# Performance work log

Measured on AMD Instinct MI355X. Metric: run time of the kernel, lower is better.

## Reference

```python
import jax, jax.numpy as jnp
import numpy as np

B, C, H, W_SP = 4, 64, 64, 64
CI = C // 2  # inter_channels = 32
DEPTH = 64
EPS = 1e-5


def conv2d(x, w, b, pad=0, dil=1):
    out = jax.lax.conv_general_dilated(
        x, w, window_strides=(1, 1),
        padding=[(pad, pad), (pad, pad)],
        rhs_dilation=(dil, dil),
        dimension_numbers=('NCHW', 'OIHW', 'NCHW'))
    return out + b[None, :, None, None]


def setup_inputs() -> dict:
    key = jax.random.key(0)
    ks = iter(jax.random.split(key, 32))
    nrm = lambda shp, s=0.01: jax.random.normal(next(ks), shp, jnp.float32) * s
    inp = {
        'x': jax.random.normal(next(ks), (B, C, H, W_SP), jnp.float32),
        # NonlocalBlock params (init: normal(0, 0.01), bias 0)
        'g_w': nrm((CI, C, 1, 1)), 'g_b': jnp.zeros((CI,), jnp.float32),
        'theta_w': nrm((CI, C, 1, 1)), 'theta_b': jnp.zeros((CI,), jnp.float32),
        'phi_w': nrm((CI, C, 1, 1)), 'phi_b': jnp.zeros((CI,), jnp.float32),
        'Wz_w': nrm((C, CI, 1, 1)), 'Wz_b': jnp.zeros((C,), jnp.float32),
        'bn_g': jax.random.normal(next(ks), (C,), jnp.float32),  # normal_(W[1].weight, 0) -> std 1
        'bn_b': jnp.zeros((C,), jnp.float32),
        # ASPP params (torch default kaiming init approximated by small normals)
        'a_mean_w': nrm((DEPTH, C, 1, 1), 0.05), 'a_mean_b': jnp.zeros((DEPTH,), jnp.float32),
        'a1_w': nrm((DEPTH, C, 1, 1), 0.05), 'a1_b': jnp.zeros((DEPTH,), jnp.float32),
        'a3_w': nrm((DEPTH, C, 3, 3), 0.02), 'a3_b': jnp.zeros((DEPTH,), jnp.float32),
        'a5_w': nrm((DEPTH, C, 3, 3), 0.02), 'a5_b': jnp.zeros((DEPTH,), jnp.float32),
        'a7_w': nrm((DEPTH, C, 3, 3), 0.02), 'a7_b': jnp.zeros((DEPTH,), jnp.float32),
        'out_w': nrm((DEPTH, DEPTH * 5, 1, 1), 0.02), 'out_b': jnp.zeros((DEPTH,), jnp.float32),
    }
    return inp


def _forward(x, g_w, g_b, theta_w, theta_b, phi_w, phi_b, Wz_w, Wz_b, bn_g, bn_b,
             a_mean_w, a_mean_b, a1_w, a1_b, a3_w, a3_b, a5_w, a5_b, a7_w, a7_b,
             out_w, out_b):
    b, c, h, w = x.shape
    n = h * w
    # ---- NonlocalBlock: global self-attention ----
    g_x = conv2d(x, g_w, g_b).reshape(b, CI, n).transpose(0, 2, 1)       # [B,N,Ci]
    theta_x = conv2d(x, theta_w, theta_b).reshape(b, CI, n).transpose(0, 2, 1)  # [B,N,Ci]
    phi_x = conv2d(x, phi_w, phi_b).reshape(b, CI, n)                    # [B,Ci,N]
    f = jnp.einsum('bqc,bck->bqk', theta_x, phi_x)                       # [B,N,N]
    f_div_C = jax.nn.softmax(f, axis=2)
    y = jnp.einsum('bqk,bkc->bqc', f_div_C, g_x)                         # [B,N,Ci]
    y = y.transpose(0, 2, 1).reshape(b, CI, h, w)
    wy = conv2d(y, Wz_w, Wz_b)
    # BatchNorm (eval: running_mean=0, running_var=1)
    wy = wy * (bn_g / jnp.sqrt(1.0 + EPS))[None, :, None, None] + bn_b[None, :, None, None]
    z = wy + x
    # ---- ASPP ----
    img = jnp.mean(z, axis=(2, 3), keepdims=True)                        # [B,C,1,1]
    img = conv2d(img, a_mean_w, a_mean_b)                                # [B,D,1,1]
    img = jnp.broadcast_to(img, (b, DEPTH, h, w))  # bilinear upsample of 1x1 is constant
    b1 = conv2d(z, a1_w, a1_b)
    b3 = conv2d(z, a3_w, a3_b, pad=3, dil=3)
    b5 = conv2d(z, a5_w, a5_b, pad=5, dil=5)
    b7 = conv2d(z, a7_w, a7_b, pad=7, dil=7)
    cat = jnp.concatenate([img, b1, b3, b5, b7], axis=1)                 # [B,5D,H,W]
    return conv2d(cat, out_w, out_b)                                     # [B,D,H,W]


def reference(x, g_w, g_b, theta_w, theta_b, phi_w, phi_b, Wz_w, Wz_b, bn_g, bn_b,
              a_mean_w, a_mean_b, a1_w, a1_b, a3_w, a3_b, a5_w, a5_b, a7_w, a7_b,
              out_w, out_b):
    return _forward(x, g_w, g_b, theta_w, theta_b, phi_w, phi_b, Wz_w, Wz_b, bn_g, bn_b,
                    a_mean_w, a_mean_b, a1_w, a1_b, a3_w, a3_b, a5_w, a5_b, a7_w, a7_b,
                    out_w, out_b)
```

## Files before the change

kernel.cpp:

```cpp
#include <hip/hip_runtime.h>


typedef __attribute__((ext_vector_type(8))) short bf16x8;
typedef __attribute__((ext_vector_type(4))) short s16x4;
typedef __attribute__((ext_vector_type(4))) float f32x4;

#define MFMA(a, b, c) __builtin_amdgcn_mfma_f32_16x16x32_bf16((a), (b), (c), 0, 0, 0)

#if __has_builtin(__builtin_amdgcn_exp2f)
#define EXP2(x) __builtin_amdgcn_exp2f(x)
#else
#define EXP2(x) exp2f(x)
#endif

__device__ static inline short f2bf(float f) {
  union { float f; unsigned u; } v; v.f = f;
  unsigned r = v.u + 0x7fffu + ((v.u >> 16) & 1u);
  return (short)(r >> 16);
}
__device__ static inline s16x4 pk4(f32x4 v) {
  s16x4 r; r.x = f2bf(v.x); r.y = f2bf(v.y); r.z = f2bf(v.z); r.w = f2bf(v.w);
  return r;
}
__device__ static inline unsigned pk2(float f0, float f1) {
  union { float f; unsigned u; } a, b; a.f = f0; b.f = f1;
  return __builtin_amdgcn_perm(b.u, a.u, 0x07060302u);
}
__device__ static inline float unlo(unsigned d) {
  union { unsigned u; float f; } v; v.u = d << 16; return v.f;
}
__device__ static inline float unhi(unsigned d) {
  union { unsigned u; float f; } v; v.u = d & 0xffff0000u; return v.f;
}
__device__ static inline unsigned fasu(float f) {
  union { float f; unsigned u; } v; v.f = f; return v.u;
}
__device__ static inline float uasf(unsigned u) {
  union { unsigned u; float f; } v; v.u = u; return v.f;
}
__device__ static inline f32x4 exp24(f32x4 v) {
  f32x4 r; r.x = EXP2(v.x); r.y = EXP2(v.y); r.z = EXP2(v.z); r.w = EXP2(v.w);
  return r;
}

#define QF_PER_B 131072
#define ZPB      389376
#define LOG2E    1.4426950408889634f

__global__ __launch_bounds__(256) void k_proj(
    const float* __restrict__ x,
    const float* __restrict__ tw, const float* __restrict__ tb,
    const float* __restrict__ pw, const float* __restrict__ pb,
    const float* __restrict__ gw, const float* __restrict__ gb,
    const float* __restrict__ Wz_w, const float* __restrict__ Wz_b,
    const float* __restrict__ bn_g, const float* __restrict__ bn_b,
    const float* __restrict__ out_w, const float* __restrict__ out_b,
    const float* __restrict__ a1_w, const float* __restrict__ a3_w,
    const float* __restrict__ a5_w, const float* __restrict__ a7_w,
    const float* __restrict__ a1_b, const float* __restrict__ a3_b,
    const float* __restrict__ a5_b, const float* __restrict__ a7_b,
    const float* __restrict__ am_w,
    unsigned short* __restrict__ thetaB, unsigned short* __restrict__ phiB,
    unsigned short* __restrict__ gB, unsigned short* __restrict__ WzF,
    float* __restrict__ bias2, float* __restrict__ zpart,
    unsigned* __restrict__ zp, unsigned short* __restrict__ Wfrag,
    float* __restrict__ am_wT, float* __restrict__ owT0,
    float* __restrict__ cbias) {
  __shared__ union {
    struct { float wlT[2048]; float bl[32]; } qkv;
    struct { float wsm[4096]; float osm[64 * 65]; } prep;
  } sm;
  int blk = blockIdx.x, t = threadIdx.x;
  if (blk < 384) {
    int proj = blk >> 7, r = blk & 127;
    int b = r & 3, pt = r >> 2;
    const float* w    = proj == 0 ? tw : (proj == 1 ? pw : gw);
    const float* bias = proj == 0 ? tb : (proj == 1 ? pb : gb);
    for (int i = t; i < 2048; i += 256)
      sm.qkv.wlT[(i & 63) * 32 + (i >> 6)] = w[i];
    if (t < 32) sm.qkv.bl[t] = bias[t];
    __syncthreads();
    int px = pt * 128 + (t & 127), tci = t >> 7;
    const float* xp = x + b*64*4096 + px;
    float acc[16];
    #pragma unroll
    for (int i = 0; i < 16; ++i) acc[i] = sm.qkv.bl[tci*16 + i];
    for (int c0 = 0; c0 < 64; c0 += 16) {
      float xv[16];
      #pragma unroll
      for (int k = 0; k < 16; ++k) xv[k] = xp[(c0 + k)*4096];
      #pragma unroll
      for (int k = 0; k < 16; ++k) {
        const float* wr = &sm.qkv.wlT[(c0 + k)*32 + tci*16];
        #pragma unroll
        for (int j = 0; j < 4; ++j) {
          f32x4 wv = *(const f32x4*)(wr + j*4);
          acc[j*4 + 0] += wv.x * xv[k];
          acc[j*4 + 1] += wv.y * xv[k];
          acc[j*4 + 2] += wv.z * xv[k];
          acc[j*4 + 3] += wv.w * xv[k];
        }
      }
    }
    if (proj == 0) {
      #pragma unroll
      for (int i = 0; i < 16; ++i) acc[i] *= LOG2E;
    }
    if (proj < 2) {
      unsigned short* base = (proj == 0 ? thetaB : phiB) + b*QF_PER_B
                             + (px >> 4)*512 + (px & 15)*8;
      #pragma unroll
      for (int qq = 0; qq < 2; ++qq) {
        bf16x8 v;
        #pragma unroll
        for (int j = 0; j < 8; ++j) v[j] = f2bf(acc[qq*8 + j]);
        *(bf16x8*)(base + (tci*2 + qq)*128) = v;
      }
    } else {
      unsigned short* base = gB + b*QF_PER_B + (px >> 5)*1024
                             + ((px & 31) >> 3)*128 + (px & 7) + tci*512;
      #pragma unroll
      for (int ci = 0; ci < 16; ++ci)
        base[ci*8] = (unsigned short)f2bf(acc[ci]);
    }
  } else if (blk == 384) {
    int ct = t >> 6, lane = t & 63, quad = lane >> 4, l15 = lane & 15;
    int c = ct * 16 + l15;
    float s = bn_g[c] * rsqrtf(1.f + 1e-5f);
    bf16x8 v;
    #pragma unroll
    for (int j = 0; j < 8; ++j) v[j] = f2bf(s * Wz_w[c * 32 + quad * 8 + j]);
    *(bf16x8*)(WzF + (ct * 64 + lane) * 8) = v;
    #pragma unroll
    for (int i = 0; i < 8; ++i) zpart[i*256 + t] = 0.f;
    if (t < 64) {
      float s2 = bn_g[t] * rsqrtf(1.f + 1e-5f);
      bias2[t] = s2 * Wz_b[t] + bn_b[t];
    }
  } else if (blk < 1381) {
    int hb = blk - 385;
    int b = hb / 249, loc = hb - b * 249;
    int i = loc * 256 + t;
    if (i >= 63616) return;
    int px = i >> 5, dw = i & 31;
    int row, col;
    if (px < 1092) {
      int r = px / 78; col = px - r * 78;
      row = (r < 7) ? r : r + 64;
    } else {
      int j = px - 1092;
      int r = j / 14; int c = j - r * 14;
      row = r + 7; col = (c < 7) ? c : c + 64;
    }
    zp[b * (ZPB / 2) + (row * 78 + col) * 32 + dw] = 0u;
  } else if (blk < 1409) {
    int tap = blk - 1381;
    const float* w; int goff, kyx = 0, ksq = 9;
    if (tap == 0)      { w = a1_w; goff = 64;  ksq = 1; }
    else if (tap < 10) { w = a3_w; goff = 128; kyx = tap - 1; }
    else if (tap < 19) { w = a5_w; goff = 192; kyx = tap - 10; }
    else               { w = a7_w; goff = 256; kyx = tap - 19; }
    for (int i = t; i < 4096; i += 256) {
      sm.prep.wsm[i] = w[i * ksq + kyx];
      int d = i >> 6, m = i & 63;
      sm.prep.osm[d * 65 + m] = out_w[d * 320 + goff + m];
    }
    __syncthreads();
    int dt = t >> 6, lane = t & 63, quad = lane >> 4, l15 = lane & 15;
    int d = dt * 16 + l15;
    float acc[16];
    #pragma unroll
    for (int k = 0; k < 16; ++k) acc[k] = 0.f;
    const float* orow = sm.prep.osm + d * 65;
    int c0 = quad * 8;
    for (int m = 0; m < 64; ++m) {
      float o = orow[m];
      const float* wr = sm.prep.wsm + m * 64 + c0;
      #pragma unroll
      for (int cc = 0; cc < 2; ++cc)
        #pragma unroll
        for (int j = 0; j < 8; ++j)
          acc[cc * 8 + j] += o * wr[cc * 32 + j];
    }
    #pragma unroll
    for (int cc = 0; cc < 2; ++cc) {
      bf16x8 v;
      #pragma unroll
      for (int j = 0; j < 8; ++j) v[j] = f2bf(acc[cc * 8 + j]);
      *(bf16x8*)(Wfrag + (((tap * 4 + dt) * 2 + cc) * 64 + lane) * 8) = v;
    }
  } else {
    for (int i = t; i < 4096; i += 256) {
      int d = i >> 6, c = i & 63;
      am_wT[c * 64 + d] = am_w[i];
      owT0[c * 64 + d] = out_w[d * 320 + c];
    }
    if (t < 64) {
      float r = out_b[t];
      const float* ow = out_w + t * 320;
      for (int m = 0; m < 64; ++m)
        r += ow[64 + m] * a1_b[m] + ow[128 + m] * a3_b[m]
           + ow[192 + m] * a5_b[m] + ow[256 + m] * a7_b[m];
      cbias[t] = r;
    }
  }
}

__global__ __launch_bounds__(512, 8) void k_attn(
    const unsigned short* __restrict__ thetaB, const unsigned short* __restrict__ phiB,
    const unsigned short* __restrict__ gB, const unsigned short* __restrict__ WzF,
    const float* __restrict__ bias2, const float* __restrict__ x,
    unsigned short* __restrict__ z_pad, float* __restrict__ zpart) {
  __shared__ struct {
    unsigned ypk[8][5][64];
    __align__(16) unsigned short plds[8][576];
  } sm;
  int blk = blockIdx.x;
  int xcd = blk & 7;
  int b = xcd >> 1;
  int qblk = ((xcd & 1) << 7) | (blk >> 3);
  int tid = threadIdx.x;
  int kh = tid >> 6, lane = tid & 63, quad = lane >> 4, l15 = lane & 15;
  const bf16x8* thB = (const bf16x8*)(thetaB + b*QF_PER_B);
  const bf16x8* phF = (const bf16x8*)(phiB + b*QF_PER_B);
  const bf16x8* gF  = (const bf16x8*)(gB + b*QF_PER_B);
  bf16x8 th = thB[qblk*64 + lane];
  bf16x8 ones;
  #pragma unroll
  for (int j = 0; j < 8; ++j) ones[j] = (short)0x3F80;
  const f32x4 z4 = {0.f, 0.f, 0.f, 0.f};
  f32x4 acc0 = z4, acc1 = z4, accL = z4;
  unsigned short* pl = &sm.plds[kh][0];
  unsigned short* rp = pl + l15*36 + quad*4;
  const unsigned short* qp = pl + l15*36 + quad*8;
  int kt0 = kh*16;
  int tb0 = kt0*128 + lane;
  bf16x8 pf0 = phF[tb0], pf1 = phF[tb0 + 64];
  for (int kt = kt0; kt < kt0 + 16; ++kt) {
    bf16x8 cp0 = pf0, cp1 = pf1;
    bf16x8 gf0 = gF[kt*128 + lane];
    bf16x8 gf1 = gF[kt*128 + lane + 64];
    if (kt + 1 < kt0 + 16) {
      int tb = (kt + 1)*128 + lane;
      pf0 = phF[tb]; pf1 = phF[tb + 64];
    }
    f32x4 s0 = MFMA(cp0, th, z4);
    f32x4 s1 = MFMA(cp1, th, z4);
    f32x4 p0 = exp24(s0), p1 = exp24(s1);
    uint2 w0; w0.x = pk2(p0.x, p0.y); w0.y = pk2(p0.z, p0.w);
    uint2 w1; w1.x = pk2(p1.x, p1.y); w1.y = pk2(p1.z, p1.w);
    *(uint2*)(rp)      = w0;
    *(uint2*)(rp + 16) = w1;
    uint2 a0 = *(const uint2*)(qp);
    uint2 a1 = *(const uint2*)(qp + 4);
    union { unsigned u[4]; bf16x8 v; } pb;
    pb.u[0] = a0.x; pb.u[1] = a0.y; pb.u[2] = a1.x; pb.u[3] = a1.y;
    acc0 = MFMA(gf0, pb.v, acc0);
    acc1 = MFMA(gf1, pb.v, acc1);
    accL = MFMA(ones, pb.v, accL);
  }
  {
    unsigned* yp = &sm.ypk[kh][0][lane];
    yp[0*64] = pk2(acc0.x, acc0.y);
    yp[1*64] = pk2(acc0.z, acc0.w);
    yp[2*64] = pk2(acc1.x, acc1.y);
    yp[3*64] = pk2(acc1.z, acc1.w);
    yp[4*64] = fasu(accL.x);
  }
  __syncthreads();
  if (kh >= 4) return;
  int ct = kh;
  f32x4 a0 = z4, a1 = z4;
  float l = 0.f;
  #pragma unroll
  for (int k = 0; k < 8; ++k) {
    const unsigned* q = &sm.ypk[k][0][lane];
    unsigned d0v = q[0], d1v = q[64], d2v = q[128], d3v = q[192];
    a0.x += unlo(d0v); a0.y += unhi(d0v); a0.z += unlo(d1v); a0.w += unhi(d1v);
    a1.x += unlo(d2v); a1.y += unhi(d2v); a1.z += unlo(d3v); a1.w += unhi(d3v);
    l += uasf(q[256]);
  }
  float rl = 1.f / l;
  a0 *= rl; a1 *= rl;
  unsigned short* yl = &sm.plds[ct][0];
  *(s16x4*)(yl + l15*36 + quad*4)      = pk4(a0);
  *(s16x4*)(yl + l15*36 + 16 + quad*4) = pk4(a1);
  bf16x8 y = *(const bf16x8*)(yl + l15*36 + quad*8);
  bf16x8 wf = ((const bf16x8*)WzF)[ct*64 + lane];
  f32x4 zq = MFMA(wf, y, z4);
  int c0 = ct*16 + quad*4;
  f32x4 b2 = *(const f32x4*)(bias2 + c0);
  int q = qblk*16 + l15;
  const float* xp = x + (b*64 + c0)*4096 + q;
  f32x4 s;
  s.x = zq.x + b2.x + xp[0];
  s.y = zq.y + b2.y + xp[4096];
  s.z = zq.z + b2.z + xp[8192];
  s.w = zq.w + b2.w + xp[12288];
  int h = q >> 6, w = q & 63;
  *(s16x4*)(z_pad + b*ZPB + ((h + 7)*78 + (w + 7))*64 + c0) = pk4(s);
  f32x4 zs = s;
  #pragma unroll
  for (int m = 1; m < 16; m <<= 1) {
    zs.x += __shfl_xor(zs.x, m);
    zs.y += __shfl_xor(zs.y, m);
    zs.z += __shfl_xor(zs.z, m);
    zs.w += __shfl_xor(zs.w, m);
  }
  if (l15 == 0) {
    float* zd = zpart + (qblk & 7)*256 + b*64 + c0;
    atomicAdd(zd + 0, zs.x);
    atomicAdd(zd + 1, zs.y);
    atomicAdd(zd + 2, zs.z);
    atomicAdd(zd + 3, zs.w);
  }
}

__global__ __launch_bounds__(256, 4) void k_conv(
    const unsigned short* __restrict__ z_pad, const unsigned short* __restrict__ Wfrag,
    const float* __restrict__ zpart, const float* __restrict__ am_wT,
    const float* __restrict__ am_b, const float* __restrict__ owT0,
    const float* __restrict__ cbias, float* __restrict__ out) {
  static constexpr int DYt[28] = {0, -3,-3,-3,0,0,0,3,3,3,
                                     -5,-5,-5,0,0,0,5,5,5,
                                     -7,-7,-7,0,0,0,7,7,7};
  static constexpr int DXt[28] = {0, -3,0,3,-3,0,3,-3,0,3,
                                     -5,0,5,-5,0,5,-5,0,5,
                                     -7,0,7,-7,0,7,-7,0,7};
  int blk = blockIdx.x;
  int xcd = blk & 7, idx = blk >> 3;
  int h = xcd*8 + (idx & 7);
  int rest = idx >> 3;
  int b = rest & 3, wh = rest >> 2;
  int tid = threadIdx.x;
  int wave = tid >> 6, lane = tid & 63, quad = lane >> 4, l15 = lane & 15;
  int dt2 = wave >> 1, cf = wave & 1;
  float zm = 0.f;
  #pragma unroll
  for (int p = 0; p < 8; ++p) zm += zpart[p*256 + b*64 + lane];
  float zml = zm * (1.f / 4096.f);
  float img = am_b[lane];
  for (int c = 0; c < 64; ++c) img += am_wT[c*64 + lane] * __shfl(zml, c);
  float cbd = cbias[lane];
  for (int dd = 0; dd < 64; ++dd) cbd += owT0[dd*64 + lane] * __shfl(img, dd);
  const unsigned short* zb = z_pad + b*ZPB + ((h + 7)*78 + 7)*64 + quad*8;
  const bf16x8* wfp = (const bf16x8*)Wfrag + lane;
  int d0 = dt2*2 + 0, d1 = dt2*2 + 1;
  const f32x4 z4 = {0.f, 0.f, 0.f, 0.f};
  f32x4 acc0 = z4, acc1 = z4;
  int col = ((wh*2 + cf)*16 + l15)*64;
  bf16x8 zq[4], wq0[4], wq1[4];
  #pragma unroll
  for (int p = 0; p < 4; ++p) {
    int tap = p >> 1, cc = p & 1;
    zq[p] = *(const bf16x8*)(zb + (DYt[tap]*78 + DXt[tap])*64 + cc*32 + col);
    wq0[p] = wfp[((tap*4 + d0)*2 + cc)*64];
    wq1[p] = wfp[((tap*4 + d1)*2 + cc)*64];
  }
  #pragma unroll
  for (int idx2 = 0; idx2 < 56; ++idx2) {
    int slot = idx2 & 3;
    bf16x8 zc = zq[slot], wc0 = wq0[slot], wc1 = wq1[slot];
    if (idx2 + 4 < 56) {
      int ntap = (idx2 + 4) >> 1, ncc = (idx2 + 4) & 1;
      zq[slot] = *(const bf16x8*)(zb + (DYt[ntap]*78 + DXt[ntap])*64 + ncc*32 + col);
      wq0[slot] = wfp[((ntap*4 + d0)*2 + ncc)*64];
      wq1[slot] = wfp[((ntap*4 + d1)*2 + ncc)*64];
    }
    acc0 = MFMA(wc0, zc, acc0);
    acc1 = MFMA(wc1, zc, acc1);
  }
  int dd0 = d0*16 + quad*4, dd1 = d1*16 + quad*4;
  f32x4 cb0v, cb1v;
  cb0v.x = __shfl(cbd, dd0 + 0); cb0v.y = __shfl(cbd, dd0 + 1);
  cb0v.z = __shfl(cbd, dd0 + 2); cb0v.w = __shfl(cbd, dd0 + 3);
  cb1v.x = __shfl(cbd, dd1 + 0); cb1v.y = __shfl(cbd, dd1 + 1);
  cb1v.z = __shfl(cbd, dd1 + 2); cb1v.w = __shfl(cbd, dd1 + 3);
  acc0 += cb0v; acc1 += cb1v;
  float* ob = out + b*262144 + h*64;
  int w0 = (wh*2 + cf)*16 + l15;
  ob[(dd0 + 0)*4096 + w0] = acc0.x;
  ob[(dd0 + 1)*4096 + w0] = acc0.y;
  ob[(dd0 + 2)*4096 + w0] = acc0.z;
  ob[(dd0 + 3)*4096 + w0] = acc0.w;
  ob[(dd1 + 0)*4096 + w0] = acc1.x;
  ob[(dd1 + 1)*4096 + w0] = acc1.y;
  ob[(dd1 + 2)*4096 + w0] = acc1.z;
  ob[(dd1 + 3)*4096 + w0] = acc1.w;
}

extern "C" void kernel_launch(void* const* d_in, const int* in_sizes, int n_in,
                              void* d_out, int out_size, void* d_ws, size_t ws_size,
                              hipStream_t stream) {
  const float* x    = (const float*)d_in[0];
  const float* g_w  = (const float*)d_in[1];
  const float* g_b  = (const float*)d_in[2];
  const float* th_w = (const float*)d_in[3];
  const float* th_b = (const float*)d_in[4];
  const float* ph_w = (const float*)d_in[5];
  const float* ph_b = (const float*)d_in[6];
  const float* Wz_w = (const float*)d_in[7];
  const float* Wz_b = (const float*)d_in[8];
  const float* bn_g = (const float*)d_in[9];
  const float* bn_b = (const float*)d_in[10];
  const float* am_w = (const float*)d_in[11];
  const float* am_b = (const float*)d_in[12];
  const float* a1_w = (const float*)d_in[13];
  const float* a1_b = (const float*)d_in[14];
  const float* a3_w = (const float*)d_in[15];
  const float* a3_b = (const float*)d_in[16];
  const float* a5_w = (const float*)d_in[17];
  const float* a5_b = (const float*)d_in[18];
  const float* a7_w = (const float*)d_in[19];
  const float* a7_b = (const float*)d_in[20];
  const float* out_w = (const float*)d_in[21];
  const float* out_b = (const float*)d_in[22];
  float* out = (float*)d_out;
  char* ws = (char*)d_ws;
  unsigned short* thetaB = (unsigned short*)(ws + 0);
  unsigned short* phiB   = (unsigned short*)(ws + 1048576);
  unsigned short* gB     = (unsigned short*)(ws + 2097152);
  unsigned short* z_pad  = (unsigned short*)(ws + 3145728);
  unsigned short* Wfrag  = (unsigned short*)(ws + 6260736);
  unsigned short* WzF    = (unsigned short*)(ws + 6490112);
  float* bias2           = (float*)(ws + 6495232);
  float* am_wT           = (float*)(ws + 6495488);
  float* owT0            = (float*)(ws + 6511872);
  float* cbias           = (float*)(ws + 6528256);
  float* zpart           = (float*)(ws + 6528512);

  k_proj<<<dim3(1410), dim3(256), 0, stream>>>(
      x, th_w, th_b, ph_w, ph_b, g_w, g_b, Wz_w, Wz_b, bn_g, bn_b,
      out_w, out_b, a1_w, a3_w, a5_w, a7_w, a1_b, a3_b, a5_b, a7_b, am_w,
      thetaB, phiB, gB, WzF, bias2, zpart,
      (unsigned*)z_pad, Wfrag, am_wT, owT0, cbias);
  k_attn<<<dim3(1024), dim3(512), 0, stream>>>(thetaB, phiB, gB, WzF, bias2, x,
                                               z_pad, zpart);
  k_conv<<<dim3(512), dim3(256), 0, stream>>>(z_pad, Wfrag, zpart, am_wT, am_b,
                                              owT0, cbias, out);
}
```

Measured before the change: 162.5 us.

## Process two query tiles per attention block to reuse phi/g fragments

Each k_attn block now handles 32 queries (two 16-query tiles) instead of 16. The loaded phi and g key fragments feed MFMAs for both tiles, which halves global key/value traffic per query, and the g loads are now software-prefetched along with phi. The grid is halved to 512 blocks, LDS buffers double, and launch bounds drop to 4 waves per SIMD. This trades lower occupancy and parallelism for higher arithmetic intensity.

```diff
diff --git a/kernel.cpp b/kernel.cpp
--- a/kernel.cpp
+++ b/kernel.cpp
@@ -206,100 +206,136 @@
   }
 }
 
-__global__ __launch_bounds__(512, 8) void k_attn(
+__global__ __launch_bounds__(512, 4) void k_attn(
     const unsigned short* __restrict__ thetaB, const unsigned short* __restrict__ phiB,
     const unsigned short* __restrict__ gB, const unsigned short* __restrict__ WzF,
     const float* __restrict__ bias2, const float* __restrict__ x,
     unsigned short* __restrict__ z_pad, float* __restrict__ zpart) {
   __shared__ struct {
-    unsigned ypk[8][5][64];
-    __align__(16) unsigned short plds[8][576];
+    unsigned ypk[8][10][64];
+    __align__(16) unsigned short plds[8][1152];
   } sm;
   int blk = blockIdx.x;
   int xcd = blk & 7;
   int b = xcd >> 1;
-  int qblk = ((xcd & 1) << 7) | (blk >> 3);
+  int qblk = ((xcd & 1) << 6) | (blk >> 3);
   int tid = threadIdx.x;
   int kh = tid >> 6, lane = tid & 63, quad = lane >> 4, l15 = lane & 15;
   const bf16x8* thB = (const bf16x8*)(thetaB + b*QF_PER_B);
   const bf16x8* phF = (const bf16x8*)(phiB + b*QF_PER_B);
   const bf16x8* gF  = (const bf16x8*)(gB + b*QF_PER_B);
-  bf16x8 th = thB[qblk*64 + lane];
+  bf16x8 th0 = thB[(qblk*2 + 0)*64 + lane];
+  bf16x8 th1 = thB[(qblk*2 + 1)*64 + lane];
   bf16x8 ones;
   #pragma unroll
   for (int j = 0; j < 8; ++j) ones[j] = (short)0x3F80;
   const f32x4 z4 = {0.f, 0.f, 0.f, 0.f};
-  f32x4 acc0 = z4, acc1 = z4, accL = z4;
+  f32x4 acc00 = z4, acc01 = z4, acc10 = z4, acc11 = z4;
+  f32x4 accL0 = z4, accL1 = z4;
   unsigned short* pl = &sm.plds[kh][0];
-  unsigned short* rp = pl + l15*36 + quad*4;
-  const unsigned short* qp = pl + l15*36 + quad*8;
+  unsigned short* r0p = pl + l15*36 + quad*4;
+  unsigned short* r1p = pl + 576 + l15*36 + quad*4;
+  const unsigned short* q0p = pl + l15*36 + quad*8;
+  const unsigned short* q1p = pl + 576 + l15*36 + quad*8;
   int kt0 = kh*16;
   int tb0 = kt0*128 + lane;
   bf16x8 pf0 = phF[tb0], pf1 = phF[tb0 + 64];
+  bf16x8 gf0 = gF[tb0],  gf1 = gF[tb0 + 64];
   for (int kt = kt0; kt < kt0 + 16; ++kt) {
-    bf16x8 cp0 = pf0, cp1 = pf1;
-    bf16x8 gf0 = gF[kt*128 + lane];
-    bf16x8 gf1 = gF[kt*128 + lane + 64];
+    bf16x8 cp0 = pf0, cp1 = pf1, cg0 = gf0, cg1 = gf1;
     if (kt + 1 < kt0 + 16) {
       int tb = (kt + 1)*128 + lane;
       pf0 = phF[tb]; pf1 = phF[tb + 64];
-    }
-    f32x4 s0 = MFMA(cp0, th, z4);
-    f32x4 s1 = MFMA(cp1, th, z4);
-    f32x4 p0 = exp24(s0), p1 = exp24(s1);
-    uint2 w0; w0.x = pk2(p0.x, p0.y); w0.y = pk2(p0.z, p0.w);
-    uint2 w1; w1.x = pk2(p1.x, p1.y); w1.y = pk2(p1.z, p1.w);
-    *(uint2*)(rp)      = w0;
-    *(uint2*)(rp + 16) = w1;
-    uint2 a0 = *(const uint2*)(qp);
-    uint2 a1 = *(const uint2*)(qp + 4);
-    union { unsigned u[4]; bf16x8 v; } pb;
-    pb.u[0] = a0.x; pb.u[1] = a0.y; pb.u[2] = a1.x; pb.u[3] = a1.y;
-    acc0 = MFMA(gf0, pb.v, acc0);
-    acc1 = MFMA(gf1, pb.v, acc1);
-    accL = MFMA(ones, pb.v, accL);
+      gf0 = gF[tb];  gf1 = gF[tb + 64];
+    }
+    f32x4 s00 = MFMA(cp0, th0, z4);
+    f32x4 s10 = MFMA(cp1, th0, z4);
+    f32x4 s01 = MFMA(cp0, th1, z4);
+    f32x4 s11 = MFMA(cp1, th1, z4);
+    f32x4 p00 = exp24(s00), p10 = exp24(s10), p01 = exp24(s01), p11 = exp24(s11);
+    uint2 w0; w0.x = pk2(p00.x, p00.y); w0.y = pk2(p00.z, p00.w);
+    uint2 w1; w1.x = pk2(p10.x, p10.y); w1.y = pk2(p10.z, p10.w);
+    uint2 w2; w2.x = pk2(p01.x, p01.y); w2.y = pk2(p01.z, p01.w);
+    uint2 w3; w3.x = pk2(p11.x, p11.y); w3.y = pk2(p11.z, p11.w);
+    *(uint2*)(r0p)      = w0;
+    *(uint2*)(r0p + 16) = w1;
+    *(uint2*)(r1p)      = w2;
+    *(uint2*)(r1p + 16) = w3;
+    uint2 a0 = *(const uint2*)(q0p);
+    uint2 a1 = *(const uint2*)(q0p + 4);
+    uint2 b0 = *(const uint2*)(q1p);
+    uint2 b1 = *(const uint2*)(q1p + 4);
+    union { unsigned u[4]; bf16x8 v; } pb0c, pb1c;
+    pb0c.u[0] = a0.x; pb0c.u[1] = a0.y; pb0c.u[2] = a1.x; pb0c.u[3] = a1.y;
+    pb1c.u[0] = b0.x; pb1c.u[1] = b0.y; pb1c.u[2] = b1.x; pb1c.u[3] = b1.y;
+    acc00 = MFMA(cg0, pb0c.v, acc00);
+    acc01 = MFMA(cg1, pb0c.v, acc01);
+    acc10 = MFMA(cg0, pb1c.v, acc10);
+    acc11 = MFMA(cg1, pb1c.v, acc11);
+    accL0 = MFMA(ones, pb0c.v, accL0);
+    accL1 = MFMA(ones, pb1c.v, accL1);
   }
   {
     unsigned* yp = &sm.ypk[kh][0][lane];
-    yp[0*64] = pk2(acc0.x, acc0.y);
-    yp[1*64] = pk2(acc0.z, acc0.w);
-    yp[2*64] = pk2(acc1.x, acc1.y);
-    yp[3*64] = pk2(acc1.z, acc1.w);
-    yp[4*64] = fasu(accL.x);
+    yp[0*64] = pk2(acc00.x, acc00.y);
+    yp[1*64] = pk2(acc00.z, acc00.w);
+    yp[2*64] = pk2(acc01.x, acc01.y);
+    yp[3*64] = pk2(acc01.z, acc01.w);
+    yp[4*64] = pk2(acc10.x, acc10.y);
+    yp[5*64] = pk2(acc10.z, acc10.w);
+    yp[6*64] = pk2(acc11.x, acc11.y);
+    yp[7*64] = pk2(acc11.z, acc11.w);
+    yp[8*64] = fasu(accL0.x);
+    yp[9*64] = fasu(accL1.x);
   }
   __syncthreads();
   if (kh >= 4) return;
   int ct = kh;
-  f32x4 a0 = z4, a1 = z4;
-  float l = 0.f;
+  f32x4 a00 = z4, a01 = z4, a10 = z4, a11 = z4;
+  float l0 = 0.f, l1 = 0.f;
   #pragma unroll
   for (int k = 0; k < 8; ++k) {
     const unsigned* q = &sm.ypk[k][0][lane];
     unsigned d0v = q[0], d1v = q[64], d2v = q[128], d3v = q[192];
-    a0.x += unlo(d0v); a0.y += unhi(d0v); a0.z += unlo(d1v); a0.w += unhi(d1v);
-    a1.x += unlo(d2v); a1.y += unhi(d2v); a1.z += unlo(d3v); a1.w += unhi(d3v);
-    l += uasf(q[256]);
-  }
-  float rl = 1.f / l;
-  a0 *= rl; a1 *= rl;
-  unsigned short* yl = &sm.plds[ct][0];
-  *(s16x4*)(yl + l15*36 + quad*4)      = pk4(a0);
-  *(s16x4*)(yl + l15*36 + 16 + quad*4) = pk4(a1);
-  bf16x8 y = *(const bf16x8*)(yl + l15*36 + quad*8);
+    unsigned d4v = q[256], d5v = q[320], d6v = q[384], d7v = q[448];
+    a00.x += unlo(d0v); a00.y += unhi(d0v); a00.z += unlo(d1v); a00.w += unhi(d1v);
+    a01.x += unlo(d2v); a01.y += unhi(d2v); a01.z += unlo(d3v); a01.w += unhi(d3v);
+    a10.x += unlo(d4v); a10.y += unhi(d4v); a10.z += unlo(d5v); a10.w += unhi(d5v);
+    a11.x += unlo(d6v); a11.y += unhi(d6v); a11.z += unlo(d7v); a11.w += unhi(d7v);
+    l0 += uasf(q[512]); l1 += uasf(q[576]);
+  }
+  float r0 = 1.f / l0, r1 = 1.f / l1;
+  a00 *= r0; a01 *= r0; a10 *= r1; a11 *= r1;
+  unsigned short* yl = &sm.plds[0][0] + ct*1280;
+  *(s16x4*)(yl + l15*40 + quad*4)             = pk4(a00);
+  *(s16x4*)(yl + l15*40 + 16 + quad*4)        = pk4(a01);
+  *(s16x4*)(yl + (16 + l15)*40 + quad*4)      = pk4(a10);
+  *(s16x4*)(yl + (16 + l15)*40 + 16 + quad*4) = pk4(a11);
+  bf16x8 y0 = *(const bf16x8*)(yl + l15*40 + quad*8);
+  bf16x8 y1 = *(const bf16x8*)(yl + (16 + l15)*40 + quad*8);
   bf16x8 wf = ((const bf16x8*)WzF)[ct*64 + lane];
-  f32x4 zq = MFMA(wf, y, z4);
+  f32x4 zq0 = MFMA(wf, y0, z4);
+  f32x4 zq1 = MFMA(wf, y1, z4);
   int c0 = ct*16 + quad*4;
   f32x4 b2 = *(const f32x4*)(bias2 + c0);
-  int q = qblk*16 + l15;
-  const float* xp = x + (b*64 + c0)*4096 + q;
-  f32x4 s;
-  s.x = zq.x + b2.x + xp[0];
-  s.y = zq.y + b2.y + xp[4096];
-  s.z = zq.z + b2.z + xp[8192];
-  s.w = zq.w + b2.w + xp[12288];
-  int h = q >> 6, w = q & 63;
-  *(s16x4*)(z_pad + b*ZPB + ((h + 7)*78 + (w + 7))*64 + c0) = pk4(s);
-  f32x4 zs = s;
+  int q0i = qblk * 32;
+  const float* xp0 = x + (b*64 + c0)*4096 + q0i + l15;
+  f32x4 s0, s1;
+  s0.x = zq0.x + b2.x + xp0[0];
+  s0.y = zq0.y + b2.y + xp0[4096];
+  s0.z = zq0.z + b2.z + xp0[8192];
+  s0.w = zq0.w + b2.w + xp0[12288];
+  s1.x = zq1.x + b2.x + xp0[16];
+  s1.y = zq1.y + b2.y + xp0[4096 + 16];
+  s1.z = zq1.z + b2.z + xp0[8192 + 16];
+  s1.w = zq1.w + b2.w + xp0[12288 + 16];
+  {
+    int q = q0i + l15, h = q >> 6, w = q & 63;
+    *(s16x4*)(z_pad + b*ZPB + ((h + 7)*78 + (w + 7))*64 + c0) = pk4(s0);
+    q = q0i + 16 + l15; h = q >> 6; w = q & 63;
+    *(s16x4*)(z_pad + b*ZPB + ((h + 7)*78 + (w + 7))*64 + c0) = pk4(s1);
+  }
+  f32x4 zs = s0 + s1;
   #pragma unroll
   for (int m = 1; m < 16; m <<= 1) {
     zs.x += __shfl_xor(zs.x, m);
@@ -434,8 +470,8 @@
       out_w, out_b, a1_w, a3_w, a5_w, a7_w, a1_b, a3_b, a5_b, a7_b, am_w,
       thetaB, phiB, gB, WzF, bias2, zpart,
       (unsigned*)z_pad, Wfrag, am_wT, owT0, cbias);
-  k_attn<<<dim3(1024), dim3(512), 0, stream>>>(thetaB, phiB, gB, WzF, bias2, x,
-                                               z_pad, zpart);
+  k_attn<<<dim3(512), dim3(512), 0, stream>>>(thetaB, phiB, gB, WzF, bias2, x,
+                                              z_pad, zpart);
   k_conv<<<dim3(512), dim3(256), 0, stream>>>(z_pad, Wfrag, zpart, am_wT, am_b,
                                               owT0, cbias, out);
 }
```

Result: faster. 157.4 us (median of 2 runs) (-3.2%).

## Process four query tiles per attention block to reuse phi and g key loads

Applied to the files above, without the earlier changes.

Each attention block now handles 64 queries (four 16-query tiles) instead of 16, so every loaded phi/g key fragment feeds four score and accumulate MFMA sets. The grid shrinks from 1024 to 256 blocks and launch bounds drop to 2 waves/SIMD to make room for the larger accumulator state. The intent is to cut global/L2 traffic for keys and values by a factor of four. In exchange, parallelism falls to 256 blocks on a 256-CU part, and register and LDS pressure rise.

```diff
diff --git a/kernel.cpp b/kernel.cpp
--- a/kernel.cpp
+++ b/kernel.cpp
@@ -206,113 +206,147 @@
   }
 }
 
-__global__ __launch_bounds__(512, 8) void k_attn(
+struct WaveBuf {
+  union {
+    __align__(16) unsigned short plds[2304];
+    unsigned ypk[20][64];
+  };
+};
+__global__ __launch_bounds__(512, 2) void k_attn(
     const unsigned short* __restrict__ thetaB, const unsigned short* __restrict__ phiB,
     const unsigned short* __restrict__ gB, const unsigned short* __restrict__ WzF,
     const float* __restrict__ bias2, const float* __restrict__ x,
     unsigned short* __restrict__ z_pad, float* __restrict__ zpart) {
   __shared__ struct {
-    unsigned ypk[8][5][64];
-    __align__(16) unsigned short plds[8][576];
+    WaveBuf w[8];
+    __align__(16) unsigned short ytr[4][2560];
   } sm;
   int blk = blockIdx.x;
   int xcd = blk & 7;
   int b = xcd >> 1;
-  int qblk = ((xcd & 1) << 7) | (blk >> 3);
+  int qblk = ((xcd & 1) << 5) | (blk >> 3);
   int tid = threadIdx.x;
   int kh = tid >> 6, lane = tid & 63, quad = lane >> 4, l15 = lane & 15;
   const bf16x8* thB = (const bf16x8*)(thetaB + b*QF_PER_B);
   const bf16x8* phF = (const bf16x8*)(phiB + b*QF_PER_B);
   const bf16x8* gF  = (const bf16x8*)(gB + b*QF_PER_B);
-  bf16x8 th = thB[qblk*64 + lane];
+  bf16x8 th[4];
+  #pragma unroll
+  for (int qt = 0; qt < 4; ++qt) th[qt] = thB[(qblk*4 + qt)*64 + lane];
   bf16x8 ones;
   #pragma unroll
   for (int j = 0; j < 8; ++j) ones[j] = (short)0x3F80;
   const f32x4 z4 = {0.f, 0.f, 0.f, 0.f};
-  f32x4 acc0 = z4, acc1 = z4, accL = z4;
-  unsigned short* pl = &sm.plds[kh][0];
-  unsigned short* rp = pl + l15*36 + quad*4;
-  const unsigned short* qp = pl + l15*36 + quad*8;
+  f32x4 acc[4][2], accL[4];
+  #pragma unroll
+  for (int qt = 0; qt < 4; ++qt) { acc[qt][0] = z4; acc[qt][1] = z4; accL[qt] = z4; }
+  unsigned short* pl = &sm.w[kh].plds[0];
   int kt0 = kh*16;
   int tb0 = kt0*128 + lane;
   bf16x8 pf0 = phF[tb0], pf1 = phF[tb0 + 64];
+  bf16x8 gf0 = gF[tb0],  gf1 = gF[tb0 + 64];
   for (int kt = kt0; kt < kt0 + 16; ++kt) {
-    bf16x8 cp0 = pf0, cp1 = pf1;
-    bf16x8 gf0 = gF[kt*128 + lane];
-    bf16x8 gf1 = gF[kt*128 + lane + 64];
+    bf16x8 cp0 = pf0, cp1 = pf1, cg0 = gf0, cg1 = gf1;
     if (kt + 1 < kt0 + 16) {
       int tb = (kt + 1)*128 + lane;
       pf0 = phF[tb]; pf1 = phF[tb + 64];
-    }
-    f32x4 s0 = MFMA(cp0, th, z4);
-    f32x4 s1 = MFMA(cp1, th, z4);
-    f32x4 p0 = exp24(s0), p1 = exp24(s1);
-    uint2 w0; w0.x = pk2(p0.x, p0.y); w0.y = pk2(p0.z, p0.w);
-    uint2 w1; w1.x = pk2(p1.x, p1.y); w1.y = pk2(p1.z, p1.w);
-    *(uint2*)(rp)      = w0;
-    *(uint2*)(rp + 16) = w1;
-    uint2 a0 = *(const uint2*)(qp);
-    uint2 a1 = *(const uint2*)(qp + 4);
-    union { unsigned u[4]; bf16x8 v; } pb;
-    pb.u[0] = a0.x; pb.u[1] = a0.y; pb.u[2] = a1.x; pb.u[3] = a1.y;
-    acc0 = MFMA(gf0, pb.v, acc0);
-    acc1 = MFMA(gf1, pb.v, acc1);
-    accL = MFMA(ones, pb.v, accL);
+      gf0 = gF[tb];  gf1 = gF[tb + 64];
+    }
+    #pragma unroll
+    for (int qt = 0; qt < 4; ++qt) {
+      f32x4 s0 = MFMA(cp0, th[qt], z4);
+      f32x4 s1 = MFMA(cp1, th[qt], z4);
+      f32x4 p0 = exp24(s0), p1 = exp24(s1);
+      uint2 w0; w0.x = pk2(p0.x, p0.y); w0.y = pk2(p0.z, p0.w);
+      uint2 w1; w1.x = pk2(p1.x, p1.y); w1.y = pk2(p1.z, p1.w);
+      unsigned short* rp = pl + qt*576 + l15*36 + quad*4;
+      *(uint2*)(rp)      = w0;
+      *(uint2*)(rp + 16) = w1;
+    }
+    #pragma unroll
+    for (int qt = 0; qt < 4; ++qt) {
+      const unsigned short* qp = pl + qt*576 + l15*36 + quad*8;
+      uint2 a0 = *(const uint2*)(qp);
+      uint2 a1 = *(const uint2*)(qp + 4);
+      union { unsigned u[4]; bf16x8 v; } pb;
+      pb.u[0] = a0.x; pb.u[1] = a0.y; pb.u[2] = a1.x; pb.u[3] = a1.y;
+      acc[qt][0] = MFMA(cg0, pb.v, acc[qt][0]);
+      acc[qt][1] = MFMA(cg1, pb.v, acc[qt][1]);
+      accL[qt]   = MFMA(ones, pb.v, accL[qt]);
+    }
   }
   {
-    unsigned* yp = &sm.ypk[kh][0][lane];
-    yp[0*64] = pk2(acc0.x, acc0.y);
-    yp[1*64] = pk2(acc0.z, acc0.w);
-    yp[2*64] = pk2(acc1.x, acc1.y);
-    yp[3*64] = pk2(acc1.z, acc1.w);
-    yp[4*64] = fasu(accL.x);
+    unsigned* yp = &sm.w[kh].ypk[0][lane];
+    #pragma unroll
+    for (int qt = 0; qt < 4; ++qt) {
+      yp[(qt*4 + 0)*64] = pk2(acc[qt][0].x, acc[qt][0].y);
+      yp[(qt*4 + 1)*64] = pk2(acc[qt][0].z, acc[qt][0].w);
+      yp[(qt*4 + 2)*64] = pk2(acc[qt][1].x, acc[qt][1].y);
+      yp[(qt*4 + 3)*64] = pk2(acc[qt][1].z, acc[qt][1].w);
+      yp[(16 + qt)*64]  = fasu(accL[qt].x);
+    }
   }
   __syncthreads();
   if (kh >= 4) return;
   int ct = kh;
-  f32x4 a0 = z4, a1 = z4;
-  float l = 0.f;
+  f32x4 a0[4], a1[4];
+  float l[4];
+  #pragma unroll
+  for (int qt = 0; qt < 4; ++qt) { a0[qt] = z4; a1[qt] = z4; l[qt] = 0.f; }
   #pragma unroll
   for (int k = 0; k < 8; ++k) {
-    const unsigned* q = &sm.ypk[k][0][lane];
-    unsigned d0v = q[0], d1v = q[64], d2v = q[128], d3v = q[192];
-    a0.x += unlo(d0v); a0.y += unhi(d0v); a0.z += unlo(d1v); a0.w += unhi(d1v);
-    a1.x += unlo(d2v); a1.y += unhi(d2v); a1.z += unlo(d3v); a1.w += unhi(d3v);
-    l += uasf(q[256]);
-  }
-  float rl = 1.f / l;
-  a0 *= rl; a1 *= rl;
-  unsigned short* yl = &sm.plds[ct][0];
-  *(s16x4*)(yl + l15*36 + quad*4)      = pk4(a0);
-  *(s16x4*)(yl + l15*36 + 16 + quad*4) = pk4(a1);
-  bf16x8 y = *(const bf16x8*)(yl + l15*36 + quad*8);
+    const unsigned* q = &sm.w[k].ypk[0][lane];
+    #pragma unroll
+    for (int qt = 0; qt < 4; ++qt) {
+      unsigned d0v = q[(qt*4 + 0)*64], d1v = q[(qt*4 + 1)*64];
+      unsigned d2v = q[(qt*4 + 2)*64], d3v = q[(qt*4 + 3)*64];
+      a0[qt].x += unlo(d0v); a0[qt].y += unhi(d0v);
+      a0[qt].z += unlo(d1v); a0[qt].w += unhi(d1v);
+      a1[qt].x += unlo(d2v); a1[qt].y += unhi(d2v);
+      a1[qt].z += unlo(d3v); a1[qt].w += unhi(d3v);
+      l[qt] += uasf(q[(16 + qt)*64]);
+    }
+  }
+  unsigned short* yl = &sm.ytr[ct][0];
+  #pragma unroll
+  for (int qt = 0; qt < 4; ++qt) {
+    float rl = 1.f / l[qt];
+    a0[qt] *= rl; a1[qt] *= rl;
+    *(s16x4*)(yl + (qt*16 + l15)*40 + quad*4)      = pk4(a0[qt]);
+    *(s16x4*)(yl + (qt*16 + l15)*40 + 16 + quad*4) = pk4(a1[qt]);
+  }
   bf16x8 wf = ((const bf16x8*)WzF)[ct*64 + lane];
-  f32x4 zq = MFMA(wf, y, z4);
   int c0 = ct*16 + quad*4;
   f32x4 b2 = *(const f32x4*)(bias2 + c0);
-  int q = qblk*16 + l15;
-  const float* xp = x + (b*64 + c0)*4096 + q;
-  f32x4 s;
-  s.x = zq.x + b2.x + xp[0];
-  s.y = zq.y + b2.y + xp[4096];
-  s.z = zq.z + b2.z + xp[8192];
-  s.w = zq.w + b2.w + xp[12288];
-  int h = q >> 6, w = q & 63;
-  *(s16x4*)(z_pad + b*ZPB + ((h + 7)*78 + (w + 7))*64 + c0) = pk4(s);
-  f32x4 zs = s;
+  f32x4 zsum = z4;
+  #pragma unroll
+  for (int qt = 0; qt < 4; ++qt) {
+    bf16x8 y = *(const bf16x8*)(yl + (qt*16 + l15)*40 + quad*8);
+    f32x4 zq = MFMA(wf, y, z4);
+    int q = qblk*64 + qt*16 + l15;
+    const float* xp = x + (b*64 + c0)*4096 + q;
+    f32x4 s;
+    s.x = zq.x + b2.x + xp[0];
+    s.y = zq.y + b2.y + xp[4096];
+    s.z = zq.z + b2.z + xp[8192];
+    s.w = zq.w + b2.w + xp[12288];
+    int h = q >> 6, w = q & 63;
+    *(s16x4*)(z_pad + b*ZPB + ((h + 7)*78 + (w + 7))*64 + c0) = pk4(s);
+    zsum += s;
+  }
   #pragma unroll
   for (int m = 1; m < 16; m <<= 1) {
-    zs.x += __shfl_xor(zs.x, m);
-    zs.y += __shfl_xor(zs.y, m);
-    zs.z += __shfl_xor(zs.z, m);
-    zs.w += __shfl_xor(zs.w, m);
+    zsum.x += __shfl_xor(zsum.x, m);
+    zsum.y += __shfl_xor(zsum.y, m);
+    zsum.z += __shfl_xor(zsum.z, m);
+    zsum.w += __shfl_xor(zsum.w, m);
   }
   if (l15 == 0) {
     float* zd = zpart + (qblk & 7)*256 + b*64 + c0;
-    atomicAdd(zd + 0, zs.x);
-    atomicAdd(zd + 1, zs.y);
-    atomicAdd(zd + 2, zs.z);
-    atomicAdd(zd + 3, zs.w);
+    atomicAdd(zd + 0, zsum.x);
+    atomicAdd(zd + 1, zsum.y);
+    atomicAdd(zd + 2, zsum.z);
+    atomicAdd(zd + 3, zsum.w);
   }
 }
 
@@ -434,8 +468,8 @@
       out_w, out_b, a1_w, a3_w, a5_w, a7_w, a1_b, a3_b, a5_b, a7_b, am_w,
       thetaB, phiB, gB, WzF, bias2, zpart,
       (unsigned*)z_pad, Wfrag, am_wT, owT0, cbias);
-  k_attn<<<dim3(1024), dim3(512), 0, stream>>>(thetaB, phiB, gB, WzF, bias2, x,
-                                               z_pad, zpart);
+  k_attn<<<dim3(256), dim3(512), 0, stream>>>(thetaB, phiB, gB, WzF, bias2, x,
+                                              z_pad, zpart);
   k_conv<<<dim3(512), dim3(256), 0, stream>>>(z_pad, Wfrag, zpart, am_wT, am_b,
                                               owT0, cbias, out);
 }
```

Result: faster. 158.5 us (-2.5%).
